# Performance work log

Hardware: AMD Instinct MI355X
Metric: run time of the kernel (lower is better)

Reference implementation:

```python
import jax, jax.numpy as jnp
import numpy as np

COEF_MEMORY = 0.2


def setup_inputs() -> dict:
    key = jax.random.key(0)
    k0, k1, k2, k3 = jax.random.split(key, 4)
    bs, T, h, w, ck, cv, M = 8, 8, 32, 32, 256, 3, 512
    return {
        "k": jax.random.normal(k0, (bs, T, h, w, ck), dtype=jnp.float32),
        "v": jax.random.normal(k1, (bs, T, h, w, cv), dtype=jnp.float32),
        "m_k": jax.random.normal(k2, (bs, T, M, ck), dtype=jnp.float32),
        "m_v": jax.random.normal(k3, (bs, T, M, cv), dtype=jnp.float32),
    }


def reference(k, v, m_k, m_v):
    # k: [bs, T, h, w, ck]; v: [bs, T, h, w, cv]
    # m_k: [bs, T, M, ck]; m_v: [bs, T, M, cv]
    bs, T, h, w, ck = k.shape
    cv = v.shape[-1]
    hw = h * w
    k_flat = k.reshape(bs, T, hw, ck)
    v_flat = v.reshape(bs, T, hw, cv)

    # queries: frame i+1 tokens; keys: frame i tokens (unscaled inner product)
    q = k_flat[:, 1:]            # [bs, T-1, hw, ck]
    ref = k_flat[:, :-1]         # [bs, T-1, hw, ck]
    sim_k = jax.nn.softmax(jnp.einsum('btqc,btkc->btqk', q, ref), axis=-1)  # [bs,T-1,hw,hw]
    recon_k = jnp.einsum('btqk,btkv->btqv', sim_k, v_flat[:, :-1])          # [bs,T-1,hw,cv]

    # frame-to-memory attention against memory at step i
    sim_m = jax.nn.softmax(jnp.einsum('btqc,btmc->btqm', q, m_k[:, :-1]), axis=-1)  # [bs,T-1,hw,M]
    recon_m = jnp.einsum('btqm,btmv->btqv', sim_m, m_v[:, :-1])                     # [bs,T-1,hw,cv]

    output_v = (1.0 - COEF_MEMORY) * recon_k + COEF_MEMORY * recon_m  # [bs,T-1,hw,cv]
    ground_truth = v[:, 1:]                                           # [bs,T-1,h,w,cv]
    return output_v, ground_truth
```

## Files before the change

kernel.cpp:

```cpp
#include <hip/hip_runtime.h>
#include <stdint.h>

typedef _Float16 f16x8 __attribute__((ext_vector_type(8)));
typedef __bf16 bf16x8 __attribute__((ext_vector_type(8)));
typedef float f32x4 __attribute__((ext_vector_type(4)));

#define MFMA_F16(a,b,c) __builtin_amdgcn_mfma_f32_16x16x32_f16(a,b,c,0,0,0)
#define MFMA_BF16(a,b,c) __builtin_amdgcn_mfma_f32_16x16x32_bf16(a,b,c,0,0,0)
#define ALPHA 1.2011224087864498f

__device__ __forceinline__ uint32_t f2u(float x){ union{float f;uint32_t u;} c; c.f=x; return c.u; }
__device__ __forceinline__ float u2f(uint32_t u){ union{float f;uint32_t u;} c; c.u=u; return c.f; }

union HU8 { uint32_t u[4]; _Float16 h[8]; f16x8 v; };

__device__ __forceinline__ void split_pair(float x0, float x1, uint32_t& hp, uint32_t& lp){
  uint32_t u0=f2u(x0), u1=f2u(x1);
  uint32_t h0=u0&0xFFFF0000u, h1=u1&0xFFFF0000u;
  hp = (u0>>16) | h1;
  float l0 = x0 - u2f(h0), l1 = x1 - u2f(h1);
  lp = (f2u(l0)>>16) | (f2u(l1)&0xFFFF0000u);
}

__device__ __forceinline__ void glds16(const void* g, void* l){
  __builtin_amdgcn_global_load_lds(
      (const __attribute__((address_space(1))) uint32_t*)(uintptr_t)g,
      (__attribute__((address_space(3))) uint32_t*)(uint32_t)(uintptr_t)l,
      16, 0, 0);
}

__global__ void kast_cvt3(const float* __restrict__ K_, const float* __restrict__ MK_,
                          uint4* __restrict__ khi, uint4* __restrict__ mkhi){
  int i = blockIdx.x*256 + threadIdx.x;
  const float* src; uint4* hi; int j;
  if (i < 2097152){ src = K_;  hi = khi;  j = i; }
  else            { src = MK_; hi = mkhi; j = i - 2097152; }
  const float4* in4 = (const float4*)src;
  float4 a = in4[(size_t)j*2], c = in4[(size_t)j*2+1];
  HU8 h;
  h.h[0]=(_Float16)(a.x*ALPHA); h.h[1]=(_Float16)(a.y*ALPHA);
  h.h[2]=(_Float16)(a.z*ALPHA); h.h[3]=(_Float16)(a.w*ALPHA);
  h.h[4]=(_Float16)(c.x*ALPHA); h.h[5]=(_Float16)(c.y*ALPHA);
  h.h[6]=(_Float16)(c.z*ALPHA); h.h[7]=(_Float16)(c.w*ALPHA);
  hi[j] = make_uint4(h.u[0],h.u[1],h.u[2],h.u[3]);
}

__launch_bounds__(256, 2)
__global__ void kast_attn12(const ushort* __restrict__ khi, const ushort* __restrict__ mkhi,
                            const float* __restrict__ V_, const float* __restrict__ MV_,
                            float* __restrict__ part) {
  __shared__ uint8_t KB[3][16384];
  __shared__ float vlds[1536];

  const int bid = blockIdx.x;
  const int xcd = bid & 7;
  const int idx = bid >> 3;
  const int grp = idx / 24;
  const int sub = idx - grp*24;
  const int s   = xcd + 8*grp;
  const int qb  = sub & 7;
  const int ks  = sub >> 3;
  const int b = s / 7, t = s % 7;

  const uint8_t* kh8; const float* vbase;
  if (ks < 2){
    size_t row0 = (size_t)((b*8 + t)*1024 + ks*512);
    kh8 = (const uint8_t*)khi + row0*512;
    vbase = V_ + row0*3;
  } else {
    size_t row0 = (size_t)((b*8 + t)*512);
    kh8 = (const uint8_t*)mkhi + row0*512;
    vbase = MV_ + row0*3;
  }

  const int tid = threadIdx.x;
  const int w = tid >> 6, l = tid & 63;
  const int lj = l & 15, lq = l >> 4;
  const int qrow0 = qb*128 + w*32;

  for (int i = tid; i < 1536; i += 256) vlds[i] = vbase[i];

  const uint8_t* q8 = (const uint8_t*)khi + (size_t)((b*8 + t + 1)*1024)*512;
  f16x8 qh[2][8];
#pragma unroll
  for (int rt=0; rt<2; rt++){
    const uint8_t* qr = q8 + (size_t)(qrow0 + rt*16 + lj)*512 + lq*16;
#pragma unroll
    for (int kc=0; kc<8; kc++)
      qh[rt][kc] = *(const f16x8*)(qr + kc*64);
  }

  float m[2][4], ssum[2][4], o[2][4][3];
#pragma unroll
  for (int rt=0;rt<2;rt++)
#pragma unroll
    for (int r=0;r<4;r++){
      m[rt][r]=-1e30f; ssum[rt][r]=0.f;
      o[rt][r][0]=0.f; o[rt][r][1]=0.f; o[rt][r][2]=0.f;
    }

  const int sg = l & 31;
  const int rsub = l >> 5;

  #define ISSUE_TILE(NT, P) do{                                              \
    _Pragma("unroll")                                                        \
    for (int i_=0;i_<4;i_++){                                                \
      int lrow_ = (w<<3) + (i_<<1) + rsub;                                   \
      size_t soff_ = (size_t)((NT)*32 + lrow_)*512 + (size_t)((sg ^ (lrow_&7))<<4); \
      uint32_t dbase_ = ((w<<3) + (i_<<1))*512;                              \
      glds16(kh8 + soff_, &KB[(P)][dbase_]);                                 \
    } }while(0)

  ISSUE_TILE(0, 0);
  ISSUE_TILE(1, 1);
  __syncthreads();

  int cur = 0, nxt = 2;
  for (int nt=0; nt<16; nt++){
    if (nt < 15){
      asm volatile("s_waitcnt vmcnt(4)" ::: "memory");
    } else {
      asm volatile("s_waitcnt vmcnt(0)" ::: "memory");
    }
    asm volatile("s_barrier" ::: "memory");

    if (nt < 14) ISSUE_TILE(nt+2, nxt);

    f32x4 acc[2][2];
#pragma unroll
    for (int rt=0;rt<2;rt++){ acc[rt][0]=(f32x4){0,0,0,0}; acc[rt][1]=(f32x4){0,0,0,0}; }

    const int sx = (l&7)<<4;
#pragma unroll
    for (int ct=0;ct<2;ct++){
      const uint8_t* rb = &KB[cur][(ct*16 + lj)*512];
#pragma unroll
      for (int kc=0;kc<8;kc++){
        int bo = (kc*64 + (lq<<4)) ^ sx;
        f16x8 bh = *(const f16x8*)(rb + bo);
        acc[0][ct] = MFMA_F16(qh[0][kc], bh, acc[0][ct]);
        acc[1][ct] = MFMA_F16(qh[1][kc], bh, acc[1][ct]);
      }
    }

    float vv[2][3];
#pragma unroll
    for (int ct=0;ct<2;ct++){
      int c = (nt*32 + ct*16 + lj)*3;
      vv[ct][0]=vlds[c]; vv[ct][1]=vlds[c+1]; vv[ct][2]=vlds[c+2];
    }
    float pm[2][4];
    float need = -1e30f;
#pragma unroll
    for (int rt=0;rt<2;rt++)
#pragma unroll
      for (int r=0;r<4;r++){
        pm[rt][r] = fmaxf(acc[rt][0][r], acc[rt][1][r]);
        need = fmaxf(need, pm[rt][r] - m[rt][r]);
      }
    if (need > 24.f){
#pragma unroll
      for (int rt=0;rt<2;rt++)
#pragma unroll
        for (int r=0;r<4;r++){
          float mn = fmaxf(m[rt][r], pm[rt][r]);
          float sc = exp2f(m[rt][r] - mn);
          ssum[rt][r] *= sc;
          o[rt][r][0] *= sc; o[rt][r][1] *= sc; o[rt][r][2] *= sc;
          m[rt][r] = mn;
        }
    }
#pragma unroll
    for (int rt=0;rt<2;rt++)
#pragma unroll
      for (int r=0;r<4;r++){
        float p0 = exp2f(acc[rt][0][r] - m[rt][r]);
        float p1 = exp2f(acc[rt][1][r] - m[rt][r]);
        ssum[rt][r] += p0 + p1;
        o[rt][r][0] += p0*vv[0][0] + p1*vv[1][0];
        o[rt][r][1] += p0*vv[0][1] + p1*vv[1][1];
        o[rt][r][2] += p0*vv[0][2] + p1*vv[1][2];
      }

    cur = (cur==2)?0:cur+1;
    nxt = (nxt==2)?0:nxt+1;
  }

#pragma unroll
  for (int rt=0;rt<2;rt++)
#pragma unroll
    for (int r=0;r<4;r++){
      float mm = m[rt][r];
      mm = fmaxf(mm, __shfl_xor(mm,1));
      mm = fmaxf(mm, __shfl_xor(mm,2));
      mm = fmaxf(mm, __shfl_xor(mm,4));
      mm = fmaxf(mm, __shfl_xor(mm,8));
      float f = exp2f(m[rt][r]-mm);
      float sl = ssum[rt][r]*f;
      float o0=o[rt][r][0]*f, o1=o[rt][r][1]*f, o2=o[rt][r][2]*f;
      sl += __shfl_xor(sl,1); sl += __shfl_xor(sl,2); sl += __shfl_xor(sl,4); sl += __shfl_xor(sl,8);
      o0 += __shfl_xor(o0,1); o0 += __shfl_xor(o0,2); o0 += __shfl_xor(o0,4); o0 += __shfl_xor(o0,8);
      o1 += __shfl_xor(o1,1); o1 += __shfl_xor(o1,2); o1 += __shfl_xor(o1,4); o1 += __shfl_xor(o1,8);
      o2 += __shfl_xor(o2,1); o2 += __shfl_xor(o2,2); o2 += __shfl_xor(o2,4); o2 += __shfl_xor(o2,8);
      if (lj == 0){
        int prow = qrow0 + rt*16 + lq*4 + r;
        float* pp = part + ((size_t)(s*3 + ks)*1024 + prow)*5;
        pp[0]=mm; pp[1]=sl; pp[2]=o0; pp[3]=o1; pp[4]=o2;
      }
    }
  #undef ISSUE_TILE
}

__global__ void kast_merge(const float* __restrict__ part, float* __restrict__ OUT_){
  int r = blockIdx.x*256 + threadIdx.x;
  if (r >= 56*1024) return;
  int s = r >> 10, row = r & 1023;
  const float* pa = part + ((size_t)(s*3+0)*1024 + row)*5;
  const float* pb = part + ((size_t)(s*3+1)*1024 + row)*5;
  const float* pm = part + ((size_t)(s*3+2)*1024 + row)*5;
  float ma=pa[0], sa=pa[1], mb=pb[0], sb=pb[1];
  float M = fmaxf(ma,mb);
  float ea = exp2f(ma-M), eb = exp2f(mb-M);
  float w1 = 0.8f / (sa*ea + sb*eb);
  float w2 = 0.2f / pm[1];
  float* op = OUT_ + (size_t)(s*1024 + row)*3;
  op[0] = (pa[2]*ea + pb[2]*eb)*w1 + pm[2]*w2;
  op[1] = (pa[3]*ea + pb[3]*eb)*w1 + pm[3]*w2;
  op[2] = (pa[4]*ea + pb[4]*eb)*w1 + pm[4]*w2;
}

__launch_bounds__(256, 2)
__global__ void kast_attn_fb(const float* __restrict__ K_, const float* __restrict__ V_,
                             const float* __restrict__ MK_, const float* __restrict__ MV_,
                             float* __restrict__ OUT_) {
  __shared__ char KhB[64*512];
  __shared__ char KlB[64*512];
  __shared__ float vlds[192];

  const int bid = blockIdx.x;
  const int s  = ((bid>>6)<<3) | (bid & 7);
  const int qb = (bid>>3) & 7;
  const int b = s / 7, t = s % 7;
  const float* qptr = K_ + (size_t)((b*8 + t + 1) * 1024) * 256;
  const float* k1   = K_ + (size_t)((b*8 + t) * 1024) * 256;
  const float* v1   = V_ + (size_t)((b*8 + t) * 1024) * 3;
  const float* k2   = MK_ + (size_t)((b*8 + t) * 512) * 256;
  const float* v2   = MV_ + (size_t)((b*8 + t) * 512) * 3;
  float* outp = OUT_ + (size_t)((b*7 + t) * 1024) * 3;

  const int tid = threadIdx.x;
  const int w = tid >> 6, l = tid & 63;
  const int lj = l & 15, lq = l >> 4;
  const int qrow0 = qb*128 + w*32;

  bf16x8 qh[2][8], ql[2][8];
#pragma unroll
  for (int rt=0; rt<2; rt++){
    const float* qr = qptr + (size_t)(qrow0 + rt*16 + lj)*256 + lq*8;
#pragma unroll
    for (int kc=0; kc<8; kc++){
      float4 a = *(const float4*)(qr + kc*32);
      float4 c = *(const float4*)(qr + kc*32 + 4);
      union { uint32_t d[4]; bf16x8 v; } hh, ll;
      split_pair(a.x, a.y, hh.d[0], ll.d[0]);
      split_pair(a.z, a.w, hh.d[1], ll.d[1]);
      split_pair(c.x, c.y, hh.d[2], ll.d[2]);
      split_pair(c.z, c.w, hh.d[3], ll.d[3]);
      qh[rt][kc]=hh.v; ql[rt][kc]=ll.v;
    }
  }

  for (int ph=0; ph<2; ph++){
    const float* ks = ph ? k2 : k1;
    const float* vs = ph ? v2 : v1;
    const int ntiles = ph ? 8 : 16;
    float m[2][4], ssum[2][4], o[2][4][3];
#pragma unroll
    for (int rt=0;rt<2;rt++)
#pragma unroll
      for (int r=0;r<4;r++){
        m[rt][r]=-1e30f; ssum[rt][r]=0.f;
        o[rt][r][0]=0.f; o[rt][r][1]=0.f; o[rt][r][2]=0.f;
      }

    for (int nt=0; nt<ntiles; nt++){
      __syncthreads();
      const float* kt = ks + (size_t)nt*64*256;
#pragma unroll 4
      for (int i=0;i<16;i++){
        int f4i = tid + i*256;
        int row = f4i >> 6;
        int col4 = f4i & 63;
        float4 x = *(const float4*)(kt + row*256 + col4*4);
        uint32_t hp0,lp0,hp1,lp1;
        split_pair(x.x,x.y,hp0,lp0);
        split_pair(x.z,x.w,hp1,lp1);
        int boff = row*512 + ((col4*8) ^ ((row&7)<<4));
        *(uint2*)(KhB + boff) = make_uint2(hp0,hp1);
        *(uint2*)(KlB + boff) = make_uint2(lp0,lp1);
      }
      if (tid < 192) vlds[tid] = vs[nt*192 + tid];
      __syncthreads();

      f32x4 acc[2][4];
#pragma unroll
      for (int rt=0;rt<2;rt++)
#pragma unroll
        for (int ct=0;ct<4;ct++)
          acc[rt][ct] = (f32x4){0.f,0.f,0.f,0.f};

      const int sx = (l&7)<<4;
#pragma unroll
      for (int ct=0;ct<4;ct++){
        const char* rbh = KhB + (ct*16 + lj)*512;
        const char* rbl = KlB + (ct*16 + lj)*512;
#pragma unroll
        for (int kc=0;kc<8;kc++){
          int bo = (kc*64 + (lq<<4)) ^ sx;
          bf16x8 bh = *(const bf16x8*)(rbh + bo);
          bf16x8 bl = *(const bf16x8*)(rbl + bo);
          acc[0][ct] = MFMA_BF16(qh[0][kc], bh, acc[0][ct]);
          acc[1][ct] = MFMA_BF16(qh[1][kc], bh, acc[1][ct]);
          acc[0][ct] = MFMA_BF16(qh[0][kc], bl, acc[0][ct]);
          acc[1][ct] = MFMA_BF16(qh[1][kc], bl, acc[1][ct]);
          acc[0][ct] = MFMA_BF16(ql[0][kc], bh, acc[0][ct]);
          acc[1][ct] = MFMA_BF16(ql[1][kc], bh, acc[1][ct]);
        }
      }

      float vv[4][3];
#pragma unroll
      for (int ct=0;ct<4;ct++){
        int c = (ct*16 + lj)*3;
        vv[ct][0]=vlds[c]; vv[ct][1]=vlds[c+1]; vv[ct][2]=vlds[c+2];
      }
#pragma unroll
      for (int rt=0;rt<2;rt++)
#pragma unroll
        for (int r=0;r<4;r++){
          float s0=acc[rt][0][r], s1=acc[rt][1][r], s2=acc[rt][2][r], s3=acc[rt][3][r];
          float tmax = fmaxf(fmaxf(s0,s1),fmaxf(s2,s3));
          float mo = m[rt][r];
          float mn = fmaxf(mo, tmax);
          float sc = __expf(mo - mn);
          float p0=__expf(s0-mn), p1=__expf(s1-mn), p2=__expf(s2-mn), p3=__expf(s3-mn);
          ssum[rt][r] = ssum[rt][r]*sc + ((p0+p1)+(p2+p3));
          o[rt][r][0] = o[rt][r][0]*sc + (p0*vv[0][0]+p1*vv[1][0]) + (p2*vv[2][0]+p3*vv[3][0]);
          o[rt][r][1] = o[rt][r][1]*sc + (p0*vv[0][1]+p1*vv[1][1]) + (p2*vv[2][1]+p3*vv[3][1]);
          o[rt][r][2] = o[rt][r][2]*sc + (p0*vv[0][2]+p1*vv[1][2]) + (p2*vv[2][2]+p3*vv[3][2]);
          m[rt][r]=mn;
        }
    }

    const float coef = ph ? 0.2f : 0.8f;
#pragma unroll
    for (int rt=0;rt<2;rt++)
#pragma unroll
      for (int r=0;r<4;r++){
        float mm = m[rt][r];
        mm = fmaxf(mm, __shfl_xor(mm,1));
        mm = fmaxf(mm, __shfl_xor(mm,2));
        mm = fmaxf(mm, __shfl_xor(mm,4));
        mm = fmaxf(mm, __shfl_xor(mm,8));
        float f = __expf(m[rt][r]-mm);
        float sl = ssum[rt][r]*f;
        float o0=o[rt][r][0]*f, o1=o[rt][r][1]*f, o2=o[rt][r][2]*f;
        sl += __shfl_xor(sl,1); sl += __shfl_xor(sl,2); sl += __shfl_xor(sl,4); sl += __shfl_xor(sl,8);
        o0 += __shfl_xor(o0,1); o0 += __shfl_xor(o0,2); o0 += __shfl_xor(o0,4); o0 += __shfl_xor(o0,8);
        o1 += __shfl_xor(o1,1); o1 += __shfl_xor(o1,2); o1 += __shfl_xor(o1,4); o1 += __shfl_xor(o1,8);
        o2 += __shfl_xor(o2,1); o2 += __shfl_xor(o2,2); o2 += __shfl_xor(o2,4); o2 += __shfl_xor(o2,8);
        if (lj == 0){
          int row = qrow0 + rt*16 + lq*4 + r;
          float* op = outp + (size_t)row*3;
          float invs = coef / sl;
          if (ph==0){ op[0]=o0*invs; op[1]=o1*invs; op[2]=o2*invs; }
          else      { op[0]+=o0*invs; op[1]+=o1*invs; op[2]+=o2*invs; }
        }
      }
  }
}

__global__ void kast_gt(const float* __restrict__ V_, float* __restrict__ OUT_){
  int s = blockIdx.x; int b = s/7, t = s%7;
  const float4* src = (const float4*)(V_ + (size_t)(b*8+t+1)*3072);
  float4* dst = (float4*)(OUT_ + 172032 + (size_t)s*3072);
  for (int i=threadIdx.x; i<768; i+=256) dst[i] = src[i];
}

extern "C" void kernel_launch(void* const* d_in, const int* in_sizes, int n_in,
                              void* d_out, int out_size, void* d_ws, size_t ws_size,
                              hipStream_t stream) {
  (void)in_sizes; (void)n_in; (void)out_size;
  const float* K_  = (const float*)d_in[0];
  const float* V_  = (const float*)d_in[1];
  const float* MK_ = (const float*)d_in[2];
  const float* MV_ = (const float*)d_in[3];
  float* out = (float*)d_out;

  const size_t NEED = 53772288;
  if (ws_size >= NEED){
    uint8_t* w8 = (uint8_t*)d_ws;
    ushort* khi  = (ushort*)(w8);
    ushort* mkhi = (ushort*)(w8 + 33554432);
    float*  part = (float*)(w8 + 50331648);
    hipLaunchKernelGGL(kast_cvt3, dim3(12288), dim3(256), 0, stream, K_, MK_,
                       (uint4*)khi, (uint4*)mkhi);
    hipLaunchKernelGGL(kast_attn12, dim3(1344), dim3(256), 0, stream, khi, mkhi, V_, MV_, part);
    hipLaunchKernelGGL(kast_merge, dim3(224),  dim3(256), 0, stream, part, out);
  } else {
    hipLaunchKernelGGL(kast_attn_fb, dim3(448), dim3(256), 0, stream, K_, V_, MK_, MV_, out);
  }
  hipLaunchKernelGGL(kast_gt, dim3(56), dim3(256), 0, stream, V_, out);
}
```

Baseline: 133.0 us.

## Split key range into six chunks per slice with double-buffered tiles

```diff
diff --git a/kernel.cpp b/kernel.cpp
--- a/kernel.cpp
+++ b/kernel.cpp
@@ -8,6 +8,7 @@
 #define MFMA_F16(a,b,c) __builtin_amdgcn_mfma_f32_16x16x32_f16(a,b,c,0,0,0)
 #define MFMA_BF16(a,b,c) __builtin_amdgcn_mfma_f32_16x16x32_bf16(a,b,c,0,0,0)
 #define ALPHA 1.2011224087864498f
+#define EXP2R(x) __builtin_amdgcn_exp2f(x)
 
 __device__ __forceinline__ uint32_t f2u(float x){ union{float f;uint32_t u;} c; c.f=x; return c.u; }
 __device__ __forceinline__ float u2f(uint32_t u){ union{float f;uint32_t u;} c; c.u=u; return c.f; }
@@ -46,29 +47,29 @@
 }
 
 __launch_bounds__(256, 2)
-__global__ void kast_attn12(const ushort* __restrict__ khi, const ushort* __restrict__ mkhi,
+__global__ void kast_attn14(const ushort* __restrict__ khi, const ushort* __restrict__ mkhi,
                             const float* __restrict__ V_, const float* __restrict__ MV_,
                             float* __restrict__ part) {
-  __shared__ uint8_t KB[3][16384];
-  __shared__ float vlds[1536];
+  __shared__ uint8_t KB[2][16384];
+  __shared__ float vlds[768];
 
   const int bid = blockIdx.x;
   const int xcd = bid & 7;
   const int idx = bid >> 3;
-  const int grp = idx / 24;
-  const int sub = idx - grp*24;
+  const int grp = idx / 48;
+  const int sub = idx - grp*48;
   const int s   = xcd + 8*grp;
   const int qb  = sub & 7;
   const int ks  = sub >> 3;
   const int b = s / 7, t = s % 7;
 
   const uint8_t* kh8; const float* vbase;
-  if (ks < 2){
-    size_t row0 = (size_t)((b*8 + t)*1024 + ks*512);
+  if (ks < 4){
+    size_t row0 = (size_t)((b*8 + t)*1024 + ks*256);
     kh8 = (const uint8_t*)khi + row0*512;
     vbase = V_ + row0*3;
   } else {
-    size_t row0 = (size_t)((b*8 + t)*512);
+    size_t row0 = (size_t)((b*8 + t)*512 + (ks-4)*256);
     kh8 = (const uint8_t*)mkhi + row0*512;
     vbase = MV_ + row0*3;
   }
@@ -78,7 +79,7 @@
   const int lj = l & 15, lq = l >> 4;
   const int qrow0 = qb*128 + w*32;
 
-  for (int i = tid; i < 1536; i += 256) vlds[i] = vbase[i];
+  for (int i = tid; i < 768; i += 256) vlds[i] = vbase[i];
 
   const uint8_t* q8 = (const uint8_t*)khi + (size_t)((b*8 + t + 1)*1024)*512;
   f16x8 qh[2][8];
@@ -112,19 +113,17 @@
     } }while(0)
 
   ISSUE_TILE(0, 0);
-  ISSUE_TILE(1, 1);
   __syncthreads();
 
-  int cur = 0, nxt = 2;
-  for (int nt=0; nt<16; nt++){
-    if (nt < 15){
+  for (int nt=0; nt<8; nt++){
+    const int cur = nt & 1;
+    if (nt < 7){
+      ISSUE_TILE(nt+1, cur^1);
       asm volatile("s_waitcnt vmcnt(4)" ::: "memory");
     } else {
       asm volatile("s_waitcnt vmcnt(0)" ::: "memory");
     }
     asm volatile("s_barrier" ::: "memory");
-
-    if (nt < 14) ISSUE_TILE(nt+2, nxt);
 
     f32x4 acc[2][2];
 #pragma unroll
@@ -164,7 +163,7 @@
 #pragma unroll
         for (int r=0;r<4;r++){
           float mn = fmaxf(m[rt][r], pm[rt][r]);
-          float sc = exp2f(m[rt][r] - mn);
+          float sc = EXP2R(m[rt][r] - mn);
           ssum[rt][r] *= sc;
           o[rt][r][0] *= sc; o[rt][r][1] *= sc; o[rt][r][2] *= sc;
           m[rt][r] = mn;
@@ -174,16 +173,15 @@
     for (int rt=0;rt<2;rt++)
 #pragma unroll
       for (int r=0;r<4;r++){
-        float p0 = exp2f(acc[rt][0][r] - m[rt][r]);
-        float p1 = exp2f(acc[rt][1][r] - m[rt][r]);
+        float p0 = EXP2R(acc[rt][0][r] - m[rt][r]);
+        float p1 = EXP2R(acc[rt][1][r] - m[rt][r]);
         ssum[rt][r] += p0 + p1;
         o[rt][r][0] += p0*vv[0][0] + p1*vv[1][0];
         o[rt][r][1] += p0*vv[0][1] + p1*vv[1][1];
         o[rt][r][2] += p0*vv[0][2] + p1*vv[1][2];
       }
 
-    cur = (cur==2)?0:cur+1;
-    nxt = (nxt==2)?0:nxt+1;
+    asm volatile("s_barrier" ::: "memory");
   }
 
 #pragma unroll
@@ -195,7 +193,7 @@
       mm = fmaxf(mm, __shfl_xor(mm,2));
       mm = fmaxf(mm, __shfl_xor(mm,4));
       mm = fmaxf(mm, __shfl_xor(mm,8));
-      float f = exp2f(m[rt][r]-mm);
+      float f = EXP2R(m[rt][r]-mm);
       float sl = ssum[rt][r]*f;
       float o0=o[rt][r][0]*f, o1=o[rt][r][1]*f, o2=o[rt][r][2]*f;
       sl += __shfl_xor(sl,1); sl += __shfl_xor(sl,2); sl += __shfl_xor(sl,4); sl += __shfl_xor(sl,8);
@@ -204,29 +202,36 @@
       o2 += __shfl_xor(o2,1); o2 += __shfl_xor(o2,2); o2 += __shfl_xor(o2,4); o2 += __shfl_xor(o2,8);
       if (lj == 0){
         int prow = qrow0 + rt*16 + lq*4 + r;
-        float* pp = part + ((size_t)(s*3 + ks)*1024 + prow)*5;
+        float* pp = part + ((size_t)(s*6 + ks)*1024 + prow)*5;
         pp[0]=mm; pp[1]=sl; pp[2]=o0; pp[3]=o1; pp[4]=o2;
       }
     }
   #undef ISSUE_TILE
 }
 
-__global__ void kast_merge(const float* __restrict__ part, float* __restrict__ OUT_){
+__global__ void kast_merge6(const float* __restrict__ part, float* __restrict__ OUT_){
   int r = blockIdx.x*256 + threadIdx.x;
   if (r >= 56*1024) return;
   int s = r >> 10, row = r & 1023;
-  const float* pa = part + ((size_t)(s*3+0)*1024 + row)*5;
-  const float* pb = part + ((size_t)(s*3+1)*1024 + row)*5;
-  const float* pm = part + ((size_t)(s*3+2)*1024 + row)*5;
-  float ma=pa[0], sa=pa[1], mb=pb[0], sb=pb[1];
-  float M = fmaxf(ma,mb);
-  float ea = exp2f(ma-M), eb = exp2f(mb-M);
-  float w1 = 0.8f / (sa*ea + sb*eb);
-  float w2 = 0.2f / pm[1];
+  const float* p[6];
+#pragma unroll
+  for (int i=0;i<6;i++) p[i] = part + ((size_t)(s*6+i)*1024 + row)*5;
+  float M1 = fmaxf(fmaxf(p[0][0], p[1][0]), fmaxf(p[2][0], p[3][0]));
+  float sK = 0.f, oK0 = 0.f, oK1 = 0.f, oK2 = 0.f;
+#pragma unroll
+  for (int i=0;i<4;i++){
+    float e = EXP2R(p[i][0]-M1);
+    sK += p[i][1]*e; oK0 += p[i][2]*e; oK1 += p[i][3]*e; oK2 += p[i][4]*e;
+  }
+  float M2 = fmaxf(p[4][0], p[5][0]);
+  float e0 = EXP2R(p[4][0]-M2), e1 = EXP2R(p[5][0]-M2);
+  float sM = p[4][1]*e0 + p[5][1]*e1;
+  float w1 = 0.8f / sK;
+  float w2 = 0.2f / sM;
   float* op = OUT_ + (size_t)(s*1024 + row)*3;
-  op[0] = (pa[2]*ea + pb[2]*eb)*w1 + pm[2]*w2;
-  op[1] = (pa[3]*ea + pb[3]*eb)*w1 + pm[3]*w2;
-  op[2] = (pa[4]*ea + pb[4]*eb)*w1 + pm[4]*w2;
+  op[0] = oK0*w1 + (p[4][2]*e0 + p[5][2]*e1)*w2;
+  op[1] = oK1*w1 + (p[4][3]*e0 + p[5][3]*e1)*w2;
+  op[2] = oK2*w1 + (p[4][4]*e0 + p[5][4]*e1)*w2;
 }
 
 __launch_bounds__(256, 2)
@@ -397,7 +402,7 @@
   const float* MV_ = (const float*)d_in[3];
   float* out = (float*)d_out;
 
-  const size_t NEED = 53772288;
+  const size_t NEED = 57212928;
   if (ws_size >= NEED){
     uint8_t* w8 = (uint8_t*)d_ws;
     ushort* khi  = (ushort*)(w8);
@@ -405,8 +410,8 @@
     float*  part = (float*)(w8 + 50331648);
     hipLaunchKernelGGL(kast_cvt3, dim3(12288), dim3(256), 0, stream, K_, MK_,
                        (uint4*)khi, (uint4*)mkhi);
-    hipLaunchKernelGGL(kast_attn12, dim3(1344), dim3(256), 0, stream, khi, mkhi, V_, MV_, part);
-    hipLaunchKernelGGL(kast_merge, dim3(224),  dim3(256), 0, stream, part, out);
+    hipLaunchKernelGGL(kast_attn14, dim3(2688), dim3(256), 0, stream, khi, mkhi, V_, MV_, part);
+    hipLaunchKernelGGL(kast_merge6, dim3(224),  dim3(256), 0, stream, part, out);
   } else {
     hipLaunchKernelGGL(kast_attn_fb, dim3(448), dim3(256), 0, stream, K_, V_, MK_, MV_, out);
   }
```

Measured after the change: 113.6 us. -14.6%, faster.
